# Kernel optimization log

Hardware: AMD Instinct MI355X
Metric: run time of the kernel (lower is better)

## Reference

```python
import jax, jax.numpy as jnp
import numpy as np
from jax import lax

T, B, E = 512, 128, 128  # timesteps, batch, embedding_size
S = 2 * T                # stack capacity: 2 pushes per step


def setup_inputs() -> dict:
    key = jax.random.key(0)
    k1, k2, k3, k4, k5 = jax.random.split(key, 5)
    return {
        "v1": jax.random.normal(k1, (T, B, E), dtype=jnp.float32),
        "v2": jax.random.normal(k2, (T, B, E), dtype=jnp.float32),
        "d1": jax.random.uniform(k3, (T, B, 1), dtype=jnp.float32),
        "d2": jax.random.uniform(k4, (T, B, 1), dtype=jnp.float32),
        "u": jax.random.uniform(k5, (T, B, 1), dtype=jnp.float32),
    }


def _step(carry, xs):
    strengths, values = carry  # [B,S], [B,S,E]; slots 0..2(t+1)-1 valid after push
    v1t, v2t, d1t, d2t, ut, t = xs  # v*: [B,E]; d*,u: [B,1]; t: scalar int
    # --- push: append two entries at the top (slots 2t, 2t+1) ---
    values = lax.dynamic_update_slice(
        values, jnp.stack([v1t, v2t], axis=1), (0, 2 * t, 0))
    strengths = lax.dynamic_update_slice(
        strengths, jnp.concatenate([d1t, d2t], axis=1), (0, 2 * t))
    # exclusive reverse cumsum = strength used above each slot (top-down order)
    rev_incl = jnp.flip(jnp.cumsum(jnp.flip(strengths, 1), axis=1), 1)  # [B,S]
    used = rev_incl - strengths  # [B,S]
    # --- read: faithful to torch.max(u - strength_used) reducing over batch ---
    m = jnp.max(ut - used, axis=0)            # [S] scalar-over-batch per slot
    w = jnp.minimum(strengths, m[None, :])    # [B,S]; invalid slots hit v=0
    summary = jnp.einsum('bs,bse->be', w, values)  # [B,E]
    # --- pop: s -= min(s, relu(u - used)) using pre-pop strengths ---
    pop_amt = jnp.minimum(strengths, jnp.maximum(0.0, ut - used))
    strengths = strengths - pop_amt
    return (strengths, values), summary


def reference(v1, v2, d1, d2, u):
    init = (jnp.zeros((B, S), v1.dtype), jnp.zeros((B, S, E), v1.dtype))
    ts = jnp.arange(T, dtype=jnp.int32)
    _, out = lax.scan(_step, init, (v1, v2, d1, d2, u, ts))
    return out  # [T,B,E]: read content at each timestep
```

## Files before the change

### kernel.cpp

```cpp
#include <hip/hip_runtime.h>
#include <cstdint>
#include <cstddef>

#define TT 512
#define BB 128
#define EE 128
#define SS 1024
#define NEG_INF (-1e30f)

typedef _Float16 half8 __attribute__((ext_vector_type(8)));
typedef float floatx4 __attribute__((ext_vector_type(4)));

__device__ __forceinline__ unsigned int pkh(float x, float y) {
    _Float16 hx = (_Float16)x, hy = (_Float16)y;
    unsigned short bx, by;
    __builtin_memcpy(&bx, &hx, 2); __builtin_memcpy(&by, &hy, 2);
    return (unsigned int)bx | ((unsigned int)by << 16);
}

__global__ __launch_bounds__(64) void prefixF(
    const float* __restrict__ d1, const float* __restrict__ d2,
    const float* __restrict__ u,
    float* __restrict__ F, float* __restrict__ Bv,
    float* __restrict__ d2T, float* __restrict__ FT,
    float* __restrict__ BvT, float* __restrict__ CST,
    float* __restrict__ CMT, float* __restrict__ HT)
{
    const int b = blockIdx.x;
    const int lane = threadIdx.x;
    const int t0 = lane * 8;

    float l1[8], l2[8], g[8];
#pragma unroll
    for (int j = 0; j < 8; ++j) {
        const int t = t0 + j;
        l1[j] = d1[t * BB + b];
        l2[j] = d2[t * BB + b];
        g[j] = u[t * BB + b] - l1[j] - l2[j];
    }
    float p[8], s = 0.f;
#pragma unroll
    for (int j = 0; j < 8; ++j) { s += g[j]; p[j] = s; }

    float v = s;
#pragma unroll
    for (int off = 1; off < 64; off <<= 1) {
        float o = __shfl_up(v, off);
        if (lane >= off) v += o;
    }
    const float excl = v - s;

    float Fv[8];
#pragma unroll
    for (int j = 0; j < 8; ++j) Fv[j] = excl + p[j];

#pragma unroll
    for (int j = 0; j < 8; ++j) {
        const int t = t0 + j;
        const float Fm1 = (j > 0) ? Fv[j - 1] : excl;
        const float Bvv = Fm1 - l1[j];
        F  [b * TT + t] = Fv[j];
        Bv [b * TT + t] = Bvv;
        d2T[b * TT + t] = l2[j];
        FT [t * BB + b] = Fv[j];
        BvT[t * BB + b] = Bvv;
    }

    float pm[8], sm[8];
    pm[0] = Fv[0];
#pragma unroll
    for (int j = 1; j < 8; ++j) pm[j] = fmaxf(pm[j - 1], Fv[j]);
    sm[7] = Fv[7];
#pragma unroll
    for (int j = 6; j >= 0; --j) sm[j] = fmaxf(sm[j + 1], Fv[j]);

    float pcar = NEG_INF, scar = NEG_INF;
#pragma unroll
    for (int off = 1; off <= 3; ++off) {
        float xu = __shfl_up(pm[7], off);
        if ((lane & 3) >= off) pcar = fmaxf(pcar, xu);
        float xd = __shfl_down(sm[0], off);
        if ((lane & 3) + off <= 3) scar = fmaxf(scar, xd);
    }

#pragma unroll
    for (int j = 0; j < 8; ++j) {
        const int t = t0 + j;
        const float Hv  = fmaxf(pcar, (j > 0) ? pm[j - 1] : NEG_INF);
        const float CSv = fmaxf(sm[j], scar);
        HT [t * BB + b] = Hv;
        CST[t * BB + b] = CSv;
    }
    if ((lane & 3) == 0)
        CMT[(lane >> 2) * BB + b] = fmaxf(sm[0], scar);
}

__global__ __launch_bounds__(256) void calcM2(
    const float* __restrict__ FT, const float* __restrict__ BvT,
    const float* __restrict__ CST, const float* __restrict__ CMT,
    const float* __restrict__ HT, const float* __restrict__ u,
    float* __restrict__ m)
{
    const int t = (int)blockIdx.y;
    const int ci = (int)blockIdx.x;
    const int ct = t >> 5;
    if (ci > ct) return;

    const int tid = threadIdx.x;
    const int b = tid & 127, h = tid >> 7;
    const int ib = 32 * ci;

    __shared__ float cand[BB][66];
    __shared__ float Tot[2][BB];
    __shared__ float red[4][64];

    const float Ft = FT[t * BB + b];

    if (ci < ct) {
        float K = HT[t * BB + b];
        for (int c = ci + 1; c < ct; ++c) K = fmaxf(K, CMT[c * BB + b]);
#pragma unroll
        for (int j = 0; j < 16; ++j) {
            const int jj = 16 * h + j;
            const int i = ib + jj;
            const float R = fmaxf(CST[i * BB + b], K);
            const float Bvv = BvT[i * BB + b];
            cand[b][2 * jj]     = Ft - fmaxf(Bvv, R);
            cand[b][2 * jj + 1] = Ft - R;
        }
    } else {
        float vv[16], sfx[16];
#pragma unroll
        for (int j = 0; j < 16; ++j) {
            const int i = ib + 16 * h + j;
            vv[j] = (i < t) ? FT[i * BB + b] : NEG_INF;
        }
        sfx[15] = vv[15];
#pragma unroll
        for (int j = 14; j >= 0; --j) sfx[j] = fmaxf(vv[j], sfx[j + 1]);
        Tot[h][b] = sfx[0];
        __syncthreads();
        const float carry = (h == 0) ? Tot[1][b] : NEG_INF;
        const float ub = u[t * BB + b];
#pragma unroll
        for (int j = 0; j < 16; ++j) {
            const int jj = 16 * h + j;
            const int i = ib + jj;
            const float R = fmaxf(sfx[j], carry);
            const float Bvv = BvT[i * BB + b];
            cand[b][2 * jj]     = Ft - fmaxf(Bvv, R);
            cand[b][2 * jj + 1] = (i == t) ? ub : (Ft - R);
        }
    }
    __syncthreads();

    {
        const int s = tid & 63, g = tid >> 6;
        float mx = NEG_INF;
        const int b0 = g * 32;
#pragma unroll 8
        for (int bb = b0; bb < b0 + 32; ++bb) mx = fmaxf(mx, cand[bb][s]);
        red[g][s] = mx;
    }
    __syncthreads();
    if (tid < 64) {
        const float r = fmaxf(fmaxf(red[0][tid], red[1][tid]),
                              fmaxf(red[2][tid], red[3][tid]));
        const int s_glob = 64 * ci + tid;
        if (s_glob < 2 * t + 2) m[(size_t)t * SS + s_glob] = r;
    }
}

#define WSO 0
#define VTO 2304
#define FRO 6912
#define S0O 7488
#define BVO 8064
#define LTO 8640
#define D2O 9088

__device__ __forceinline__ float tileQ(const float* Lt, int lo, int hi) {
    const int len = hi - lo + 1;
    const int j = 31 - __builtin_clz(len);
    return fmaxf(Lt[j * 64 + lo], Lt[j * 64 + hi + 1 - (1 << j)]);
}

__global__ __launch_bounds__(256) void phaseC_mfma(
    const float* __restrict__ F, const float* __restrict__ Bvg,
    const float* __restrict__ d2T, const float* __restrict__ m,
    const float* __restrict__ v1, const float* __restrict__ v2,
    float* __restrict__ out)
{
    const int b  = blockIdx.x & (BB - 1);
    const int k8 = blockIdx.x >> 7;
    const int tt = 7 - (k8 ^ (((k8 + 2) >> 2) & 1));
    const int t0 = tt * 64;
    const int tid = threadIdx.x;

    __shared__ float sh[9152];

    const int lane = tid & 63, w = tid >> 6;
    const int wr = w >> 1, wc = w & 1;
    const int n = lane & 15;
    const int kq = (lane >> 4) * 8;
    const int il = tid & 31, g = tid >> 5;
    const int veb = tid & 7;
    const int vip = ((tid >> 3) & 7) + 8 * wc;
    const int veh = wr * 64;
    const float* Lt = &sh[LTO];
    const int nchunks = 2 * tt + 2;

    float4 pv[8];
    float2 pmv[8];

    auto prefetch = [&](int ck) {
        const int ib = 32 * ck;
        const int i = ib + il;
#pragma unroll
        for (int r8 = 0; r8 < 8; ++r8) {
            const int t = t0 + 8 * g + r8;
            pmv[r8] = *(const float2*)&m[(size_t)t * SS + 2 * i];
        }
        const int i0 = ib + 2 * vip, i1 = i0 + 1;
        const float* p10 = v1 + ((size_t)i0 * BB + b) * EE;
        const float* p11 = v1 + ((size_t)i1 * BB + b) * EE;
        const float* p20 = v2 + ((size_t)i0 * BB + b) * EE;
        const float* p21 = v2 + ((size_t)i1 * BB + b) * EE;
#pragma unroll
        for (int c = 0; c < 2; ++c) {
            const int e0 = 4 * veb + 32 * c + veh;
            pv[4 * c + 0] = *(const float4*)&p10[e0];
            pv[4 * c + 1] = *(const float4*)&p11[e0];
            pv[4 * c + 2] = *(const float4*)&p20[e0];
            pv[4 * c + 3] = *(const float4*)&p21[e0];
        }
    };

    const int nF = t0 + 64;
    for (int k = tid; k < nF; k += 256) {
        sh[FRO + k] = F[b * TT + k];
        sh[BVO + k] = Bvg[b * TT + k];
    }
    if (tid < 64) sh[D2O + tid] = d2T[b * TT + t0 + tid];

    prefetch(0);

    __syncthreads();

    {
        const int k1 = tid, k2 = tid + 256, k3 = tid + 512;
        sh[S0O + k1] = (k1 < t0) ? sh[FRO + k1] : NEG_INF;
        sh[S0O + k2] = (k2 < t0) ? sh[FRO + k2] : NEG_INF;
        if (k3 < 576) sh[S0O + k3] = NEG_INF;
        if (tid < 64) sh[LTO + tid] = sh[FRO + t0 + tid];
        __syncthreads();
        for (int off = 1; off < t0; off <<= 1) {
            float a1 = sh[S0O + k1]; if (k1 + off < 576) a1 = fmaxf(a1, sh[S0O + k1 + off]);
            float a2 = sh[S0O + k2]; if (k2 + off < 576) a2 = fmaxf(a2, sh[S0O + k2 + off]);
            __syncthreads();
            sh[S0O + k1] = a1; sh[S0O + k2] = a2;
            __syncthreads();
        }
        for (int j = 1; j < 7; ++j) {
            float v = 0.f;
            if (tid < 64)
                v = fmaxf(sh[LTO + (j - 1) * 64 + tid],
                          sh[LTO + (j - 1) * 64 + min(tid + (1 << (j - 1)), 63)]);
            __syncthreads();
            if (tid < 64) sh[LTO + j * 64 + tid] = v;
            __syncthreads();
        }
    }

    floatx4 acc[2][4];
#pragma unroll
    for (int r = 0; r < 2; ++r)
#pragma unroll
        for (int j = 0; j < 4; ++j) acc[r][j] = (floatx4)0.f;

    for (int ck = 0; ck < nchunks; ++ck) {
        const int ib = 32 * ck;

        unsigned int wreg[8];
        {
            const int i = ib + il;
            const float Ai = (i > 0) ? sh[FRO + i - 1] : 0.f;
            const float Bi = sh[BVO + i];
            const bool below = (i < t0);
            const float S0i = below ? sh[S0O + i] : 0.f;
#pragma unroll
            for (int r8 = 0; r8 < 8; ++r8) {
                const int t_l = 8 * g + r8;
                const int t = t0 + t_l;
                float w0 = 0.f, w1 = 0.f;
                if (i <= t) {
                    float R;
                    if (below) {
                        const float qq = (t_l > 0) ? tileQ(Lt, 0, t_l - 1) : NEG_INF;
                        R = fmaxf(S0i, qq);
                    } else {
                        const int li = i - t0;
                        R = (t_l - 1 >= li) ? tileQ(Lt, li, t_l - 1) : NEG_INF;
                    }
                    const float2 mv = pmv[r8];
                    const float a0 = fmaxf(Ai, R) - fmaxf(Bi, R);
                    const float a1 = (i == t) ? sh[D2O + t_l] : fmaxf(Bi - R, 0.f);
                    w0 = fminf(a0, mv.x);
                    w1 = fminf(a1, mv.y);
                }
                wreg[r8] = pkh(w0, w1);
            }
        }

        uint2 vreg[8];
#pragma unroll
        for (int c = 0; c < 2; ++c) {
            const float4 xa = pv[4 * c + 0], xb = pv[4 * c + 1];
            const float4 ya = pv[4 * c + 2], yb = pv[4 * c + 3];
            vreg[4 * c + 0] = make_uint2(pkh(xa.x, ya.x), pkh(xb.x, yb.x));
            vreg[4 * c + 1] = make_uint2(pkh(xa.y, ya.y), pkh(xb.y, yb.y));
            vreg[4 * c + 2] = make_uint2(pkh(xa.z, ya.z), pkh(xb.z, yb.z));
            vreg[4 * c + 3] = make_uint2(pkh(xa.w, ya.w), pkh(xb.w, yb.w));
        }

        __syncthreads();

#pragma unroll
        for (int r8 = 0; r8 < 8; ++r8)
            ((unsigned int*)sh)[(8 * g + r8) * 36 + il] = wreg[r8];
        {
            unsigned int* vt = (unsigned int*)sh + VTO;
            const int dw = 2 * vip;
#pragma unroll
            for (int c = 0; c < 2; ++c) {
                const int e0 = 4 * veb + 32 * c + veh;
                *(uint2*)&vt[(e0 + 0) * 36 + dw] = vreg[4 * c + 0];
                *(uint2*)&vt[(e0 + 1) * 36 + dw] = vreg[4 * c + 1];
                *(uint2*)&vt[(e0 + 2) * 36 + dw] = vreg[4 * c + 2];
                *(uint2*)&vt[(e0 + 3) * 36 + dw] = vreg[4 * c + 3];
            }
        }

        __syncthreads();

        if (ck + 1 < nchunks) prefetch(ck + 1);

        __builtin_amdgcn_s_setprio(1);
        {
            const _Float16* WsH = (const _Float16*)sh;
            const _Float16* VtH = (const _Float16*)(sh + VTO);
#pragma unroll
            for (int k2 = 0; k2 < 64; k2 += 32) {
                const half8 av0 = *(const half8*)&WsH[(32 * wr + n) * 72 + kq + k2];
                const half8 av1 = *(const half8*)&WsH[(32 * wr + 16 + n) * 72 + kq + k2];
#pragma unroll
                for (int j = 0; j < 4; ++j) {
                    const half8 bv = *(const half8*)&VtH[(64 * wc + 16 * j + n) * 72 + kq + k2];
                    acc[0][j] = __builtin_amdgcn_mfma_f32_16x16x32_f16(av0, bv, acc[0][j], 0, 0, 0);
                    acc[1][j] = __builtin_amdgcn_mfma_f32_16x16x32_f16(av1, bv, acc[1][j], 0, 0, 0);
                }
            }
        }
        __builtin_amdgcn_s_setprio(0);
    }

    {
        const int q = lane >> 4;
#pragma unroll
        for (int r = 0; r < 2; ++r) {
#pragma unroll
            for (int j = 0; j < 4; ++j) {
#pragma unroll
                for (int reg = 0; reg < 4; ++reg) {
                    const int t = t0 + 32 * wr + 16 * r + 4 * q + reg;
                    const int col = 64 * wc + 16 * j + n;
                    out[((size_t)t * BB + b) * EE + col] = acc[r][j][reg];
                }
            }
        }
    }
}

extern "C" void kernel_launch(void* const* d_in, const int* in_sizes, int n_in,
                              void* d_out, int out_size, void* d_ws, size_t ws_size,
                              hipStream_t stream) {
    const float* v1 = (const float*)d_in[0];
    const float* v2 = (const float*)d_in[1];
    const float* d1 = (const float*)d_in[2];
    const float* d2 = (const float*)d_in[3];
    const float* u  = (const float*)d_in[4];
    float* out = (float*)d_out;

    char* ws = (char*)d_ws;
    float* m   = (float*)ws;
    float* F   = m   + (size_t)TT * SS;
    float* Bvp = F   + (size_t)BB * TT;
    float* d2T = Bvp + (size_t)BB * TT;
    float* FT  = d2T + (size_t)BB * TT;
    float* BvT = FT  + (size_t)BB * TT;
    float* CST = BvT + (size_t)BB * TT;
    float* HT  = CST + (size_t)BB * TT;
    float* CMT = HT  + (size_t)BB * TT;

    prefixF<<<dim3(BB), dim3(64), 0, stream>>>(d1, d2, u, F, Bvp, d2T, FT,
                                               BvT, CST, CMT, HT);
    calcM2 <<<dim3(16, TT), dim3(256), 0, stream>>>(FT, BvT, CST, CMT, HT, u, m);
    phaseC_mfma<<<dim3(BB * 8), dim3(256), 0, stream>>>(F, Bvp, d2T, m, v1, v2, out);
}
```

Measured before the change: 200.9 us.

## Rewrite m computation with per-timestep blocks and register batch reduction

Replaces calcM2, which used a 2D grid of (chunk, t) blocks, each writing a 128x64 candidate tile to shared memory and reducing it over batch with syncs. The new calcM4 uses one block per timestep, launched in reverse order so the largest timesteps start first. Each lane owns one slot index and loops over batch, broadcasting per-batch scalars with readlane and keeping running maxima in registers. Prefix outputs are now stored batch-major, which drops the transposed BvT buffer. The diagonal group runs a 6-step shuffle suffix-max for every one of the 128 batch iterations, and this serial work could offset the savings.

```diff
diff --git a/kernel.cpp b/kernel.cpp
--- a/kernel.cpp
+++ b/kernel.cpp
@@ -18,13 +18,17 @@
     return (unsigned int)bx | ((unsigned int)by << 16);
 }
 
+__device__ __forceinline__ float rdlane(float x, int l) {
+    return __int_as_float(__builtin_amdgcn_readlane(__float_as_int(x), l));
+}
+
 __global__ __launch_bounds__(64) void prefixF(
     const float* __restrict__ d1, const float* __restrict__ d2,
     const float* __restrict__ u,
     float* __restrict__ F, float* __restrict__ Bv,
     float* __restrict__ d2T, float* __restrict__ FT,
-    float* __restrict__ BvT, float* __restrict__ CST,
-    float* __restrict__ CMT, float* __restrict__ HT)
+    float* __restrict__ CSb, float* __restrict__ CMT,
+    float* __restrict__ HT)
 {
     const int b = blockIdx.x;
     const int lane = threadIdx.x;
@@ -63,7 +67,6 @@
         Bv [b * TT + t] = Bvv;
         d2T[b * TT + t] = l2[j];
         FT [t * BB + b] = Fv[j];
-        BvT[t * BB + b] = Bvv;
     }
 
     float pm[8], sm[8];
@@ -89,85 +92,98 @@
         const float Hv  = fmaxf(pcar, (j > 0) ? pm[j - 1] : NEG_INF);
         const float CSv = fmaxf(sm[j], scar);
         HT [t * BB + b] = Hv;
-        CST[t * BB + b] = CSv;
+        CSb[b * TT + t] = CSv;
     }
     if ((lane & 3) == 0)
         CMT[(lane >> 2) * BB + b] = fmaxf(sm[0], scar);
 }
 
-__global__ __launch_bounds__(256) void calcM2(
-    const float* __restrict__ FT, const float* __restrict__ BvT,
-    const float* __restrict__ CST, const float* __restrict__ CMT,
-    const float* __restrict__ HT, const float* __restrict__ u,
+__global__ __launch_bounds__(256) void calcM4(
+    const float* __restrict__ Fb,
+    const float* __restrict__ Bvb,
+    const float* __restrict__ CSb,
+    const float* __restrict__ FT,
+    const float* __restrict__ CMT,
+    const float* __restrict__ HT,
+    const float* __restrict__ u,
     float* __restrict__ m)
 {
-    const int t = (int)blockIdx.y;
-    const int ci = (int)blockIdx.x;
+    const int t = (TT - 1) - (int)blockIdx.x;
+    const int tid = threadIdx.x;
+    const int w = tid >> 6, lane = tid & 63;
     const int ct = t >> 5;
-    if (ci > ct) return;
-
-    const int tid = threadIdx.x;
-    const int b = tid & 127, h = tid >> 7;
-    const int ib = 32 * ci;
-
-    __shared__ float cand[BB][66];
-    __shared__ float Tot[2][BB];
-    __shared__ float red[4][64];
-
-    const float Ft = FT[t * BB + b];
-
-    if (ci < ct) {
-        float K = HT[t * BB + b];
-        for (int c = ci + 1; c < ct; ++c) K = fmaxf(K, CMT[c * BB + b]);
-#pragma unroll
-        for (int j = 0; j < 16; ++j) {
-            const int jj = 16 * h + j;
-            const int i = ib + jj;
-            const float R = fmaxf(CST[i * BB + b], K);
-            const float Bvv = BvT[i * BB + b];
-            cand[b][2 * jj]     = Ft - fmaxf(Bvv, R);
-            cand[b][2 * jj + 1] = Ft - R;
-        }
-    } else {
-        float vv[16], sfx[16];
-#pragma unroll
-        for (int j = 0; j < 16; ++j) {
-            const int i = ib + 16 * h + j;
-            vv[j] = (i < t) ? FT[i * BB + b] : NEG_INF;
-        }
-        sfx[15] = vv[15];
-#pragma unroll
-        for (int j = 14; j >= 0; --j) sfx[j] = fmaxf(vv[j], sfx[j + 1]);
-        Tot[h][b] = sfx[0];
-        __syncthreads();
-        const float carry = (h == 0) ? Tot[1][b] : NEG_INF;
-        const float ub = u[t * BB + b];
-#pragma unroll
-        for (int j = 0; j < 16; ++j) {
-            const int jj = 16 * h + j;
-            const int i = ib + jj;
-            const float R = fmaxf(sfx[j], carry);
-            const float Bvv = BvT[i * BB + b];
-            cand[b][2 * jj]     = Ft - fmaxf(Bvv, R);
-            cand[b][2 * jj + 1] = (i == t) ? ub : (Ft - R);
-        }
-    }
-    __syncthreads();
-
-    {
-        const int s = tid & 63, g = tid >> 6;
-        float mx = NEG_INF;
-        const int b0 = g * 32;
-#pragma unroll 8
-        for (int bb = b0; bb < b0 + 32; ++bb) mx = fmaxf(mx, cand[bb][s]);
-        red[g][s] = mx;
-    }
-    __syncthreads();
-    if (tid < 64) {
-        const float r = fmaxf(fmaxf(red[0][tid], red[1][tid]),
-                              fmaxf(red[2][tid], red[3][tid]));
-        const int s_glob = 64 * ci + tid;
-        if (s_glob < 2 * t + 2) m[(size_t)t * SS + s_glob] = r;
+    const int ngroups = (t >> 6) + 1;
+
+    const float Ft_a = FT[t * BB + lane],      Ft_b = FT[t * BB + 64 + lane];
+    const float u_a  = u [t * BB + lane],      u_b  = u [t * BB + 64 + lane];
+    const float H_a  = HT[t * BB + lane],      H_b  = HT[t * BB + 64 + lane];
+
+    for (int g = w; g < ngroups; g += 4) {
+        const int i = (g << 6) + lane;
+        const bool diagGrp = (g == ngroups - 1);
+        const bool upper = (lane >= 32);
+
+        float K0a = H_a, K0b = H_b, K1a = H_a, K1b = H_b;
+        for (int c = 2 * g + 1; c < ct; ++c) {
+            const float ma = CMT[c * BB + lane];
+            const float mb = CMT[c * BB + 64 + lane];
+            K0a = fmaxf(K0a, ma); K0b = fmaxf(K0b, mb);
+            if (c > 2 * g + 1) { K1a = fmaxf(K1a, ma); K1b = fmaxf(K1b, mb); }
+        }
+
+        float acc0 = NEG_INF, acc1 = NEG_INF;
+        const float* csp = CSb + i;
+        const float* bvp = Bvb + i;
+        const float* fbp = Fb  + i;
+
+        if (!diagGrp) {
+#pragma unroll 4
+            for (int b = 0; b < 64; ++b) {
+                const float cs = csp[b * TT];
+                const float bv = bvp[b * TT];
+                const float Kc  = upper ? rdlane(K1a, b) : rdlane(K0a, b);
+                const float Fts = rdlane(Ft_a, b);
+                const float R = fmaxf(cs, Kc);
+                acc0 = fmaxf(acc0, Fts - fmaxf(bv, R));
+                acc1 = fmaxf(acc1, Fts - R);
+            }
+#pragma unroll 4
+            for (int b = 0; b < 64; ++b) {
+                const float cs = csp[(b + 64) * TT];
+                const float bv = bvp[(b + 64) * TT];
+                const float Kc  = upper ? rdlane(K1b, b) : rdlane(K0b, b);
+                const float Fts = rdlane(Ft_b, b);
+                const float R = fmaxf(cs, Kc);
+                acc0 = fmaxf(acc0, Fts - fmaxf(bv, R));
+                acc1 = fmaxf(acc1, Fts - R);
+            }
+        } else {
+            const bool isDiag = ((i >> 5) == ct);
+#pragma unroll 2
+            for (int bo = 0; bo < 128; ++bo) {
+                const bool lo = (bo < 64);
+                const int bl = lo ? bo : bo - 64;
+                const float cs = csp[bo * TT];
+                const float bv = bvp[bo * TT];
+                const float fl = fbp[bo * TT];
+                const float Kc  = upper ? (lo ? rdlane(K1a, bl) : rdlane(K1b, bl))
+                                        : (lo ? rdlane(K0a, bl) : rdlane(K0b, bl));
+                const float Fts = lo ? rdlane(Ft_a, bl) : rdlane(Ft_b, bl);
+                const float us  = lo ? rdlane(u_a, bl)  : rdlane(u_b, bl);
+                float x = (i < t) ? fl : NEG_INF;
+#pragma unroll
+                for (int off = 1; off < 64; off <<= 1) {
+                    const float y = __shfl_down(x, off);
+                    if (lane + off < 64) x = fmaxf(x, y);
+                }
+                const float R = isDiag ? x : fmaxf(cs, Kc);
+                acc0 = fmaxf(acc0, Fts - fmaxf(bv, R));
+                acc1 = fmaxf(acc1, (i == t) ? us : (Fts - R));
+            }
+        }
+
+        if (i <= t)
+            *(float2*)&m[(size_t)t * SS + 2 * i] = make_float2(acc0, acc1);
     }
 }
 
@@ -397,13 +413,12 @@
     float* Bvp = F   + (size_t)BB * TT;
     float* d2T = Bvp + (size_t)BB * TT;
     float* FT  = d2T + (size_t)BB * TT;
-    float* BvT = FT  + (size_t)BB * TT;
-    float* CST = BvT + (size_t)BB * TT;
-    float* HT  = CST + (size_t)BB * TT;
+    float* CSb = FT  + (size_t)BB * TT;
+    float* HT  = CSb + (size_t)BB * TT;
     float* CMT = HT  + (size_t)BB * TT;
 
     prefixF<<<dim3(BB), dim3(64), 0, stream>>>(d1, d2, u, F, Bvp, d2T, FT,
-                                               BvT, CST, CMT, HT);
-    calcM2 <<<dim3(16, TT), dim3(256), 0, stream>>>(FT, BvT, CST, CMT, HT, u, m);
+                                               CSb, CMT, HT);
+    calcM4 <<<dim3(TT), dim3(256), 0, stream>>>(F, Bvp, CSb, FT, CMT, HT, u, m);
     phaseC_mfma<<<dim3(BB * 8), dim3(256), 0, stream>>>(F, Bvp, d2T, m, v1, v2, out);
 }
```

Result: slower. 229.0 us (+14.0%).

## Replace sparse-table range max with running prefix max, shrink LDS padding, use cvt_pkrtz

Applied to the files above, without the earlier changes.

Removes the per-block sparse table used for range-max queries. Each thread now keeps a running max over its 8 timesteps in registers, seeded with a wave-shuffle exclusive prefix max for below-tile chunks and a short loop for diagonal chunks. This drops six barrier-separated table-build steps and two LDS lookups per weight element. The LDS row pitch shrinks from 72 to 68 halves, which may change bank-conflict behaviour. Value packing switches to the hardware round-toward-zero pack instruction, which alters rounding slightly.

```diff
diff --git a/kernel.cpp b/kernel.cpp
--- a/kernel.cpp
+++ b/kernel.cpp
@@ -16,6 +16,11 @@
     unsigned short bx, by;
     __builtin_memcpy(&bx, &hx, 2); __builtin_memcpy(&by, &hy, 2);
     return (unsigned int)bx | ((unsigned int)by << 16);
+}
+
+__device__ __forceinline__ unsigned int pkrtz(float x, float y) {
+    auto h = __builtin_amdgcn_cvt_pkrtz(x, y);
+    unsigned int r; __builtin_memcpy(&r, &h, 4); return r;
 }
 
 __global__ __launch_bounds__(64) void prefixF(
@@ -171,19 +176,14 @@
     }
 }
 
-#define WSO 0
-#define VTO 2304
-#define FRO 6912
-#define S0O 7488
-#define BVO 8064
-#define LTO 8640
-#define D2O 9088
-
-__device__ __forceinline__ float tileQ(const float* Lt, int lo, int hi) {
-    const int len = hi - lo + 1;
-    const int j = 31 - __builtin_clz(len);
-    return fmaxf(Lt[j * 64 + lo], Lt[j * 64 + hi + 1 - (1 << j)]);
-}
+#define PWH 68
+#define PWW 34
+#define VTO 2176
+#define FRO 6528
+#define S0O 7040
+#define BVO 7616
+#define D2O 8128
+#define TPO 8192
 
 __global__ __launch_bounds__(256) void phaseC_mfma(
     const float* __restrict__ F, const float* __restrict__ Bvg,
@@ -197,7 +197,7 @@
     const int t0 = tt * 64;
     const int tid = threadIdx.x;
 
-    __shared__ float sh[9152];
+    __shared__ float sh[8256];
 
     const int lane = tid & 63, w = tid >> 6;
     const int wr = w >> 1, wc = w & 1;
@@ -207,7 +207,6 @@
     const int veb = tid & 7;
     const int vip = ((tid >> 3) & 7) + 8 * wc;
     const int veh = wr * 64;
-    const float* Lt = &sh[LTO];
     const int nchunks = 2 * tt + 2;
 
     float4 pv[8];
@@ -252,7 +251,16 @@
         sh[S0O + k1] = (k1 < t0) ? sh[FRO + k1] : NEG_INF;
         sh[S0O + k2] = (k2 < t0) ? sh[FRO + k2] : NEG_INF;
         if (k3 < 576) sh[S0O + k3] = NEG_INF;
-        if (tid < 64) sh[LTO + tid] = sh[FRO + t0 + tid];
+        if (tid < 64) {
+            float xi = sh[FRO + t0 + tid];
+#pragma unroll
+            for (int off = 1; off < 64; off <<= 1) {
+                const float y = __shfl_up(xi, off);
+                if (tid >= off) xi = fmaxf(xi, y);
+            }
+            const float ex = __shfl_up(xi, 1);
+            sh[TPO + tid] = (tid == 0) ? NEG_INF : ex;
+        }
         __syncthreads();
         for (int off = 1; off < t0; off <<= 1) {
             float a1 = sh[S0O + k1]; if (k1 + off < 576) a1 = fmaxf(a1, sh[S0O + k1 + off]);
@@ -261,16 +269,12 @@
             sh[S0O + k1] = a1; sh[S0O + k2] = a2;
             __syncthreads();
         }
-        for (int j = 1; j < 7; ++j) {
-            float v = 0.f;
-            if (tid < 64)
-                v = fmaxf(sh[LTO + (j - 1) * 64 + tid],
-                          sh[LTO + (j - 1) * 64 + min(tid + (1 << (j - 1)), 63)]);
-            __syncthreads();
-            if (tid < 64) sh[LTO + j * 64 + tid] = v;
-            __syncthreads();
-        }
-    }
+    }
+
+    float Freg2[8];
+#pragma unroll
+    for (int j = 0; j < 8; ++j) Freg2[j] = sh[FRO + t0 + 8 * g + j];
+    const float qstart = sh[TPO + 8 * g];
 
     floatx4 acc[2][4];
 #pragma unroll
@@ -280,33 +284,45 @@
 
     for (int ck = 0; ck < nchunks; ++ck) {
         const int ib = 32 * ck;
+        const int i = ib + il;
+        const bool below = (ib < t0);
 
         unsigned int wreg[8];
         {
-            const int i = ib + il;
             const float Ai = (i > 0) ? sh[FRO + i - 1] : 0.f;
             const float Bi = sh[BVO + i];
-            const bool below = (i < t0);
-            const float S0i = below ? sh[S0O + i] : 0.f;
+            const int li = i - t0;
+            float q, S0i = 0.f;
+            if (below) {
+                S0i = sh[S0O + i];
+                q = qstart;
+            } else {
+                q = NEG_INF;
+                for (int k = li; k < 8 * g; ++k)
+                    q = fmaxf(q, sh[FRO + t0 + k]);
+            }
 #pragma unroll
             for (int r8 = 0; r8 < 8; ++r8) {
                 const int t_l = 8 * g + r8;
-                const int t = t0 + t_l;
+                const float2 mv = pmv[r8];
                 float w0 = 0.f, w1 = 0.f;
-                if (i <= t) {
-                    float R;
-                    if (below) {
-                        const float qq = (t_l > 0) ? tileQ(Lt, 0, t_l - 1) : NEG_INF;
-                        R = fmaxf(S0i, qq);
-                    } else {
-                        const int li = i - t0;
-                        R = (t_l - 1 >= li) ? tileQ(Lt, li, t_l - 1) : NEG_INF;
-                    }
-                    const float2 mv = pmv[r8];
+                if (below) {
+                    const float R = fmaxf(S0i, q);
                     const float a0 = fmaxf(Ai, R) - fmaxf(Bi, R);
-                    const float a1 = (i == t) ? sh[D2O + t_l] : fmaxf(Bi - R, 0.f);
+                    const float a1 = fmaxf(Bi - R, 0.f);
                     w0 = fminf(a0, mv.x);
                     w1 = fminf(a1, mv.y);
+                    q = fmaxf(q, Freg2[r8]);
+                } else {
+                    if (li <= t_l) {
+                        const float R = q;
+                        const float a0 = fmaxf(Ai, R) - fmaxf(Bi, R);
+                        const float a1 = (li == t_l) ? sh[D2O + t_l]
+                                                     : fmaxf(Bi - R, 0.f);
+                        w0 = fminf(a0, mv.x);
+                        w1 = fminf(a1, mv.y);
+                    }
+                    q = fmaxf(q, (t_l >= li) ? Freg2[r8] : NEG_INF);
                 }
                 wreg[r8] = pkh(w0, w1);
             }
@@ -317,27 +333,27 @@
         for (int c = 0; c < 2; ++c) {
             const float4 xa = pv[4 * c + 0], xb = pv[4 * c + 1];
             const float4 ya = pv[4 * c + 2], yb = pv[4 * c + 3];
-            vreg[4 * c + 0] = make_uint2(pkh(xa.x, ya.x), pkh(xb.x, yb.x));
-            vreg[4 * c + 1] = make_uint2(pkh(xa.y, ya.y), pkh(xb.y, yb.y));
-            vreg[4 * c + 2] = make_uint2(pkh(xa.z, ya.z), pkh(xb.z, yb.z));
-            vreg[4 * c + 3] = make_uint2(pkh(xa.w, ya.w), pkh(xb.w, yb.w));
+            vreg[4 * c + 0] = make_uint2(pkrtz(xa.x, ya.x), pkrtz(xb.x, yb.x));
+            vreg[4 * c + 1] = make_uint2(pkrtz(xa.y, ya.y), pkrtz(xb.y, yb.y));
+            vreg[4 * c + 2] = make_uint2(pkrtz(xa.z, ya.z), pkrtz(xb.z, yb.z));
+            vreg[4 * c + 3] = make_uint2(pkrtz(xa.w, ya.w), pkrtz(xb.w, yb.w));
         }
 
         __syncthreads();
 
 #pragma unroll
         for (int r8 = 0; r8 < 8; ++r8)
-            ((unsigned int*)sh)[(8 * g + r8) * 36 + il] = wreg[r8];
+            ((unsigned int*)sh)[(8 * g + r8) * PWW + il] = wreg[r8];
         {
             unsigned int* vt = (unsigned int*)sh + VTO;
             const int dw = 2 * vip;
 #pragma unroll
             for (int c = 0; c < 2; ++c) {
                 const int e0 = 4 * veb + 32 * c + veh;
-                *(uint2*)&vt[(e0 + 0) * 36 + dw] = vreg[4 * c + 0];
-                *(uint2*)&vt[(e0 + 1) * 36 + dw] = vreg[4 * c + 1];
-                *(uint2*)&vt[(e0 + 2) * 36 + dw] = vreg[4 * c + 2];
-                *(uint2*)&vt[(e0 + 3) * 36 + dw] = vreg[4 * c + 3];
+                *(uint2*)&vt[(e0 + 0) * PWW + dw] = vreg[4 * c + 0];
+                *(uint2*)&vt[(e0 + 1) * PWW + dw] = vreg[4 * c + 1];
+                *(uint2*)&vt[(e0 + 2) * PWW + dw] = vreg[4 * c + 2];
+                *(uint2*)&vt[(e0 + 3) * PWW + dw] = vreg[4 * c + 3];
             }
         }
 
@@ -351,11 +367,11 @@
             const _Float16* VtH = (const _Float16*)(sh + VTO);
 #pragma unroll
             for (int k2 = 0; k2 < 64; k2 += 32) {
-                const half8 av0 = *(const half8*)&WsH[(32 * wr + n) * 72 + kq + k2];
-                const half8 av1 = *(const half8*)&WsH[(32 * wr + 16 + n) * 72 + kq + k2];
+                const half8 av0 = *(const half8*)&WsH[(32 * wr + n) * PWH + kq + k2];
+                const half8 av1 = *(const half8*)&WsH[(32 * wr + 16 + n) * PWH + kq + k2];
 #pragma unroll
                 for (int j = 0; j < 4; ++j) {
-                    const half8 bv = *(const half8*)&VtH[(64 * wc + 16 * j + n) * 72 + kq + k2];
+                    const half8 bv = *(const half8*)&VtH[(64 * wc + 16 * j + n) * PWH + kq + k2];
                     acc[0][j] = __builtin_amdgcn_mfma_f32_16x16x32_f16(av0, bv, acc[0][j], 0, 0, 0);
                     acc[1][j] = __builtin_amdgcn_mfma_f32_16x16x32_f16(av1, bv, acc[1][j], 0, 0, 0);
                 }
```

New measurement: 226.6 us. 12.8% more time.
